# Optimization experiments

Hardware: AMD Instinct MI355X
Metric: run time of the kernel (lower is better)

Reference implementation:

```python
import jax, jax.numpy as jnp
import numpy as np

B, N, F_IN = 2, 2048, 256
HEADS, F_OUT = 8, 32
NEG_SLOPE = 0.01  # torch F.leaky_relu default


def setup_inputs() -> dict:
    key = jax.random.key(0)
    k1, k2, k3, k4 = jax.random.split(key, 4)
    stdv = 1.0 / np.sqrt(F_OUT * HEADS)
    h = jax.random.normal(k1, (B, N, F_IN), dtype=jnp.float32)
    adj = jax.random.uniform(k2, (B, N, N), dtype=jnp.float32)
    W = jax.random.normal(k3, (F_IN, F_OUT * HEADS), dtype=jnp.float32) * stdv
    a = jax.random.normal(k4, (2 * F_OUT, 1), dtype=jnp.float32) * stdv
    return {"h": h, "adj": adj, "W": W, "a": a}


def reference(h, adj, W, a):
    # adj is accepted by the original forward but never used (dense attention).
    b, n, _ = h.shape
    f = a.shape[0] // 2
    heads = W.shape[1] // f
    Wh = (h @ W).reshape(b, n, heads, f)            # [b,n,h,f]
    a1 = a[:f, 0]                                    # attends to source i
    a2 = a[f:, 0]                                    # attends to target j
    e1 = jnp.einsum('bnhf,f->bhn', Wh, a1)           # [b,h,n]
    e2 = jnp.einsum('bnhf,f->bhn', Wh, a2)           # [b,h,n]
    # e[b,h,i,j] = leaky_relu(a1.Wh_i + a2.Wh_j) == a^T [Wh_i || Wh_j]
    e = jax.nn.leaky_relu(e1[:, :, :, None] + e2[:, :, None, :], NEG_SLOPE)
    att = jax.nn.softmax(e, axis=-1)                 # softmax over neighbors j
    h_prime = jnp.einsum('bhij,bjhf->bihf', att, Wh)  # [b,n,h,f]
    return h_prime.reshape(b, n, heads * f)
```

## Files before the change

kernel.cpp:

```cpp
#include <hip/hip_runtime.h>
#include <math.h>

#define BATCH 2
#define NTOK  2048
#define FIN   256
#define HEADS 8
#define FOUT  32
#define BH    (BATCH*HEADS)
#define NCOL  (HEADS*FOUT)
#define ROWS  (BATCH*NTOK)

static const size_t OFF_E1   = 1048576;
static const size_t OFF_E2   = OFF_E1 + 32768;
static const size_t OFF_SKEY = OFF_E2 + 32768;
static const size_t OFF_SIDX = OFF_SKEY + 32768;
static const size_t OFF_W1S  = OFF_SIDX + 32768;
static const size_t OFF_W2S  = OFF_W1S + 32768;
static const size_t OFF_S1   = OFF_W2S + 32768;
static const size_t OFF_P2   = OFF_S1 + 32784;
static const size_t OFF_V1   = OFF_P2 + 32784;
static const size_t OFF_P2V  = OFF_V1 + 16u*2049u*32u;
static const size_t OFF_PART = OFF_V1;

__global__ __launch_bounds__(256) void k_gemm(const float* __restrict__ h,
                                              const float* __restrict__ W,
                                              float* __restrict__ Wh) {
    __shared__ float As[32 * 68];
    __shared__ float Bs[64 * 68];
    const int tid  = threadIdx.x;
    const int row0 = blockIdx.x * 32;
    const int col0 = blockIdx.y * 64;
    const int tc = tid & 15;
    const int tr = tid >> 4;
    const int r0 = tr * 2;

    const float4* h4 = (const float4*)h;
    const float4* W4 = (const float4*)W;

    float4 acc0 = make_float4(0.f,0.f,0.f,0.f);
    float4 acc1 = make_float4(0.f,0.f,0.f,0.f);

    for (int kc = 0; kc < FIN; kc += 64) {
        #pragma unroll
        for (int q = 0; q < 2; ++q) {
            int idx = q * 256 + tid;
            int r  = idx >> 4;
            int kq = idx & 15;
            float4 v = h4[(size_t)(row0 + r) * 64 + (kc >> 2) + kq];
            *(float4*)&As[r * 68 + kq * 4] = v;
        }
        #pragma unroll
        for (int q = 0; q < 4; ++q) {
            int idx = q * 256 + tid;
            int kr = idx >> 4;
            int cf = idx & 15;
            float4 v = W4[(size_t)(kc + kr) * 64 + (col0 >> 2) + cf];
            *(float4*)&Bs[kr * 68 + cf * 4] = v;
        }
        __syncthreads();

        #pragma unroll
        for (int kq = 0; kq < 16; ++kq) {
            float4 af0 = *(const float4*)&As[r0 * 68 + kq * 4];
            float4 af1 = *(const float4*)&As[(r0 + 1) * 68 + kq * 4];
            #pragma unroll
            for (int c = 0; c < 4; ++c) {
                float4 b = *(const float4*)&Bs[(kq * 4 + c) * 68 + tc * 4];
                float a0 = (c == 0) ? af0.x : (c == 1) ? af0.y : (c == 2) ? af0.z : af0.w;
                float a1 = (c == 0) ? af1.x : (c == 1) ? af1.y : (c == 2) ? af1.z : af1.w;
                acc0.x += a0 * b.x; acc0.y += a0 * b.y; acc0.z += a0 * b.z; acc0.w += a0 * b.w;
                acc1.x += a1 * b.x; acc1.y += a1 * b.y; acc1.z += a1 * b.z; acc1.w += a1 * b.w;
            }
        }
        __syncthreads();
    }
    *(float4*)(Wh + (size_t)(row0 + r0)     * NCOL + col0 + tc * 4) = acc0;
    *(float4*)(Wh + (size_t)(row0 + r0 + 1) * NCOL + col0 + tc * 4) = acc1;
}

__global__ __launch_bounds__(256) void k_e12(const float* __restrict__ Wh,
                                             const float* __restrict__ a,
                                             float* __restrict__ e1,
                                             float* __restrict__ e2) {
    __shared__ float av[64];
    const int tid = threadIdx.x;
    if (tid < 64) av[tid] = a[tid];
    __syncthreads();

    const int g     = blockIdx.x * 256 + tid;
    const int n_lin = g >> 3;
    const int hh    = g & 7;
    const float4* p = (const float4*)(Wh + (size_t)n_lin * NCOL + hh * FOUT);
    float s1 = 0.f, s2 = 0.f;
    #pragma unroll
    for (int q = 0; q < 8; ++q) {
        float4 v = p[q];
        s1 += v.x * av[q*4+0] + v.y * av[q*4+1] + v.z * av[q*4+2] + v.w * av[q*4+3];
        s2 += v.x * av[32+q*4+0] + v.y * av[32+q*4+1] + v.z * av[32+q*4+2] + v.w * av[32+q*4+3];
    }
    const int b  = n_lin >> 11;
    const int n  = n_lin & (NTOK - 1);
    const int bh = b * HEADS + hh;
    e1[bh * NTOK + n] = s1;
    e2[bh * NTOK + n] = s2;
}

__global__ __launch_bounds__(256) void k_rank8(const float* __restrict__ e2g,
                                               int* __restrict__ partial) {
    __shared__ float ch[256];
    const int tid = threadIdx.x;
    const int bh  = blockIdx.x;
    const int jt  = blockIdx.y;
    const int kt  = blockIdx.z;
    ch[tid] = e2g[bh * NTOK + kt * 256 + tid];
    __syncthreads();

    const int j    = jt * 256 + tid;
    const float my = e2g[bh * NTOK + j];
    const int base0 = kt * 256;
    int rank = 0;
    const float4* c4 = (const float4*)ch;
    #pragma unroll 8
    for (int q = 0; q < 64; ++q) {
        float4 v = c4[q];
        int bb = base0 + q * 4;
        rank += (v.x > my) || ((v.x == my) && (bb + 0 < j));
        rank += (v.y > my) || ((v.y == my) && (bb + 1 < j));
        rank += (v.z > my) || ((v.z == my) && (bb + 2 < j));
        rank += (v.w > my) || ((v.w == my) && (bb + 3 < j));
    }
    partial[(kt * BH + bh) * NTOK + j] = rank;
}

__global__ __launch_bounds__(256) void k_scatter(const float* __restrict__ e2g,
                                                 const int* __restrict__ partial,
                                                 float* __restrict__ skey,
                                                 int* __restrict__ sidx,
                                                 float* __restrict__ w1s,
                                                 float* __restrict__ w2s) {
    const int tid = threadIdx.x;
    const int bh  = blockIdx.x;
    const int jt  = blockIdx.y;
    const int j   = jt * 256 + tid;
    int rank = 0;
    #pragma unroll
    for (int kt = 0; kt < 8; ++kt)
        rank += partial[(kt * BH + bh) * NTOK + j];
    const float my = e2g[bh * NTOK + j];
    skey[bh * NTOK + rank] = my;
    sidx[bh * NTOK + rank] = j;
    w1s[bh * NTOK + rank]  = expf(my);
    w2s[bh * NTOK + rank]  = expf(0.01f * my);
}

__global__ __launch_bounds__(1024) void k_vscan(const float* __restrict__ Wh,
                                                const int* __restrict__ sidx,
                                                const float* __restrict__ w1s,
                                                const float* __restrict__ w2s,
                                                float* __restrict__ V1,
                                                float* __restrict__ P2V,
                                                float* __restrict__ S1,
                                                float* __restrict__ P2) {
    __shared__ float4 wtot[16];
    __shared__ float4 woff[16];
    const int t    = threadIdx.x;
    const int lane = t & 63;
    const int wv   = t >> 6;
    const int fg   = blockIdx.x;
    const int bh   = blockIdx.y;
    const int z    = blockIdx.z;
    const int b    = bh >> 3;
    const int hh   = bh & 7;
    const float* wsrc = z ? w2s : w1s;

    const int j0 = 2 * t;
    float4 v0, v1;
    if (fg < 8) {
        int sj0 = sidx[bh * NTOK + j0];
        int sj1 = sidx[bh * NTOK + j0 + 1];
        float w0 = wsrc[bh * NTOK + j0];
        float w1 = wsrc[bh * NTOK + j0 + 1];
        float4 g0 = *(const float4*)(Wh + (size_t)(b * NTOK + sj0) * NCOL + hh * FOUT + fg * 4);
        float4 g1 = *(const float4*)(Wh + (size_t)(b * NTOK + sj1) * NCOL + hh * FOUT + fg * 4);
        v0 = make_float4(w0 * g0.x, w0 * g0.y, w0 * g0.z, w0 * g0.w);
        v1 = make_float4(w1 * g1.x, w1 * g1.y, w1 * g1.z, w1 * g1.w);
    } else {
        v0 = make_float4(wsrc[bh * NTOK + j0],     0.f, 0.f, 0.f);
        v1 = make_float4(wsrc[bh * NTOK + j0 + 1], 0.f, 0.f, 0.f);
    }

    float4 s = make_float4(v0.x + v1.x, v0.y + v1.y, v0.z + v1.z, v0.w + v1.w);
    #pragma unroll
    for (int d = 1; d < 64; d <<= 1) {
        float ux = __shfl_up(s.x, (unsigned)d, 64);
        float uy = __shfl_up(s.y, (unsigned)d, 64);
        float uz = __shfl_up(s.z, (unsigned)d, 64);
        float uw = __shfl_up(s.w, (unsigned)d, 64);
        if (lane >= d) { s.x += ux; s.y += uy; s.z += uz; s.w += uw; }
    }
    float4 pair = make_float4(v0.x + v1.x, v0.y + v1.y, v0.z + v1.z, v0.w + v1.w);
    float4 excl = make_float4(s.x - pair.x, s.y - pair.y, s.z - pair.z, s.w - pair.w);
    if (lane == 63) wtot[wv] = s;
    __syncthreads();
    if (t < 16) {
        float4 ws = wtot[t];
        float4 inc = ws;
        #pragma unroll
        for (int d = 1; d < 16; d <<= 1) {
            float ux = __shfl_up(inc.x, (unsigned)d, 16);
            float uy = __shfl_up(inc.y, (unsigned)d, 16);
            float uz = __shfl_up(inc.z, (unsigned)d, 16);
            float uw = __shfl_up(inc.w, (unsigned)d, 16);
            if ((t & 15) >= d) { inc.x += ux; inc.y += uy; inc.z += uz; inc.w += uw; }
        }
        woff[t] = make_float4(inc.x - ws.x, inc.y - ws.y, inc.z - ws.z, inc.w - ws.w);
    }
    __syncthreads();

    float4 base = woff[wv];
    float4 i0 = make_float4(base.x + excl.x + v0.x, base.y + excl.y + v0.y,
                            base.z + excl.z + v0.z, base.w + excl.w + v0.w);
    float4 i1 = make_float4(i0.x + v1.x, i0.y + v1.y, i0.z + v1.z, i0.w + v1.w);

    if (fg < 8) {
        float* dst = z ? P2V : V1;
        *(float4*)(dst + ((size_t)bh * 2049 + (j0 + 1)) * 32 + fg * 4) = i0;
        *(float4*)(dst + ((size_t)bh * 2049 + (j0 + 2)) * 32 + fg * 4) = i1;
        if (t == 0)
            *(float4*)(dst + ((size_t)bh * 2049) * 32 + fg * 4) = make_float4(0.f,0.f,0.f,0.f);
    } else {
        float* dst = z ? P2 : S1;
        dst[bh * 2049 + j0 + 1] = i0.x;
        dst[bh * 2049 + j0 + 2] = i1.x;
        if (t == 0) dst[bh * 2049] = 0.f;
    }
}

__global__ __launch_bounds__(256) void k_out(const float* __restrict__ skey,
                                             const float* __restrict__ e1g,
                                             const float* __restrict__ S1,
                                             const float* __restrict__ P2,
                                             const float* __restrict__ V1,
                                             const float* __restrict__ P2V,
                                             float* __restrict__ out) {
    __shared__ float keys[NTOK];
    const int tid = threadIdx.x;
    const int it  = blockIdx.x;
    const int bh  = blockIdx.y;
    const int b   = bh >> 3;
    const int hh  = bh & 7;
    #pragma unroll
    for (int q = 0; q < 8; ++q)
        keys[q * 256 + tid] = skey[bh * NTOK + q * 256 + tid];
    __syncthreads();

    const int i  = it * 32 + (tid >> 3);
    const int fg = tid & 7;
    const float e1v = e1g[bh * NTOK + i];
    const float th  = -e1v;
    int lo = 0, hi = NTOK;
    while (lo < hi) {
        int mid = (lo + hi) >> 1;
        if (keys[mid] > th) lo = mid + 1; else hi = mid;
    }
    const int k = lo;
    const float A = expf(e1v);
    const float C = expf(0.01f * e1v);
    const float s1  = S1[bh * 2049 + k];
    const float p2k = P2[bh * 2049 + k];
    const float p2t = P2[bh * 2049 + 2048];
    const float l   = A * s1 + C * (p2t - p2k);
    const float inv = 1.0f / l;
    float4 v1   = *(const float4*)(V1  + ((size_t)bh * 2049 + k)    * 32 + fg * 4);
    float4 p2v  = *(const float4*)(P2V + ((size_t)bh * 2049 + k)    * 32 + fg * 4);
    float4 p2vt = *(const float4*)(P2V + ((size_t)bh * 2049 + 2048) * 32 + fg * 4);
    float4 o;
    o.x = (A * v1.x + C * (p2vt.x - p2v.x)) * inv;
    o.y = (A * v1.y + C * (p2vt.y - p2v.y)) * inv;
    o.z = (A * v1.z + C * (p2vt.z - p2v.z)) * inv;
    o.w = (A * v1.w + C * (p2vt.w - p2v.w)) * inv;
    *(float4*)(out + (size_t)(b * NTOK + i) * NCOL + hh * FOUT + fg * 4) = o;
}

extern "C" void kernel_launch(void* const* d_in, const int* in_sizes, int n_in,
                              void* d_out, int out_size, void* d_ws, size_t ws_size,
                              hipStream_t stream) {
    const float* h = (const float*)d_in[0];
    const float* W = (const float*)d_in[2];
    const float* a = (const float*)d_in[3];
    float* out = (float*)d_out;
    float* ws  = (float*)d_ws;

    float* Wh   = ws;
    float* e1   = ws + OFF_E1;
    float* e2   = ws + OFF_E2;
    float* skey = ws + OFF_SKEY;
    int*   sidx = (int*)(ws + OFF_SIDX);
    float* w1s  = ws + OFF_W1S;
    float* w2s  = ws + OFF_W2S;
    float* S1   = ws + OFF_S1;
    float* P2   = ws + OFF_P2;
    float* V1   = ws + OFF_V1;
    float* P2V  = ws + OFF_P2V;
    int*   part = (int*)(ws + OFF_PART);

    k_gemm   <<<dim3(ROWS / 32, NCOL / 64), 256, 0, stream>>>(h, W, Wh);
    k_e12    <<<dim3(ROWS * HEADS / 256),   256, 0, stream>>>(Wh, a, e1, e2);
    k_rank8  <<<dim3(BH, 8, 8),             256, 0, stream>>>(e2, part);
    k_scatter<<<dim3(BH, 8),                256, 0, stream>>>(e2, part, skey, sidx, w1s, w2s);
    k_vscan  <<<dim3(9, BH, 2),            1024, 0, stream>>>(Wh, sidx, w1s, w2s, V1, P2V, S1, P2);
    k_out    <<<dim3(NTOK / 32, BH),        256, 0, stream>>>(skey, e1, S1, P2, V1, P2V, out);
}
```

Baseline: 126.9 us.

## Double-buffer 64x64 GEMM tiles, use packed 64-bit sort keys, split prefix planes

The projection GEMM now uses 64x64 output tiles with a 4x4 register micro-tile per thread, a transposed A tile in shared memory and double-buffered register prefetch. This raises arithmetic reuse and halves the number of barriers per k-step. The rank kernel packs each float key and its index into one order-preserving 64-bit integer, so every comparison is a single compare instead of a compare plus tie-break. The V1/P2V prefix arrays are stored as per-feature-group planes, which changes the gather pattern in the output kernel. The risks are more register pressure and 64-bit compare cost in the rank loop.

New measurement: 122.1 us. -3.8%, faster.

```diff
diff --git a/kernel.cpp b/kernel.cpp
--- a/kernel.cpp
+++ b/kernel.cpp
@@ -25,57 +25,67 @@
 __global__ __launch_bounds__(256) void k_gemm(const float* __restrict__ h,
                                               const float* __restrict__ W,
                                               float* __restrict__ Wh) {
-    __shared__ float As[32 * 68];
-    __shared__ float Bs[64 * 68];
+    __shared__ alignas(16) float As[2][32][68];
+    __shared__ alignas(16) float Bs[2][32][72];
     const int tid  = threadIdx.x;
-    const int row0 = blockIdx.x * 32;
+    const int row0 = blockIdx.x * 64;
     const int col0 = blockIdx.y * 64;
-    const int tc = tid & 15;
-    const int tr = tid >> 4;
-    const int r0 = tr * 2;
-
-    const float4* h4 = (const float4*)h;
-    const float4* W4 = (const float4*)W;
+    const int tx   = tid & 15;
+    const int ty   = tid >> 4;
+    const int ar   = tid >> 3;
+    const int akq  = tid & 7;
+    const int bkr  = tid >> 4;
+    const int bcf  = tid & 15;
+    const int colf = col0 >> 2;
+
+    const float4* __restrict__ h4 = (const float4*)h;
+    const float4* __restrict__ W4 = (const float4*)W;
+
+    float4 a0 = h4[(size_t)(row0 + ar)      * 64 + akq];
+    float4 a1 = h4[(size_t)(row0 + 32 + ar) * 64 + akq];
+    float4 b0 = W4[(size_t)(bkr)      * 64 + colf + bcf];
+    float4 b1 = W4[(size_t)(16 + bkr) * 64 + colf + bcf];
 
     float4 acc0 = make_float4(0.f,0.f,0.f,0.f);
     float4 acc1 = make_float4(0.f,0.f,0.f,0.f);
-
-    for (int kc = 0; kc < FIN; kc += 64) {
-        #pragma unroll
-        for (int q = 0; q < 2; ++q) {
-            int idx = q * 256 + tid;
-            int r  = idx >> 4;
-            int kq = idx & 15;
-            float4 v = h4[(size_t)(row0 + r) * 64 + (kc >> 2) + kq];
-            *(float4*)&As[r * 68 + kq * 4] = v;
+    float4 acc2 = make_float4(0.f,0.f,0.f,0.f);
+    float4 acc3 = make_float4(0.f,0.f,0.f,0.f);
+
+    for (int t = 0; t < FIN / 32; ++t) {
+        const int cur = t & 1;
+        As[cur][akq*4+0][ar]      = a0.x;
+        As[cur][akq*4+1][ar]      = a0.y;
+        As[cur][akq*4+2][ar]      = a0.z;
+        As[cur][akq*4+3][ar]      = a0.w;
+        As[cur][akq*4+0][32 + ar] = a1.x;
+        As[cur][akq*4+1][32 + ar] = a1.y;
+        As[cur][akq*4+2][32 + ar] = a1.z;
+        As[cur][akq*4+3][32 + ar] = a1.w;
+        *(float4*)&Bs[cur][bkr][bcf*4]      = b0;
+        *(float4*)&Bs[cur][16 + bkr][bcf*4] = b1;
+        __syncthreads();
+        if (t + 1 < FIN / 32) {
+            const int kc = (t + 1) * 32;
+            a0 = h4[(size_t)(row0 + ar)      * 64 + (kc >> 2) + akq];
+            a1 = h4[(size_t)(row0 + 32 + ar) * 64 + (kc >> 2) + akq];
+            b0 = W4[(size_t)(kc + bkr)      * 64 + colf + bcf];
+            b1 = W4[(size_t)(kc + 16 + bkr) * 64 + colf + bcf];
         }
         #pragma unroll
-        for (int q = 0; q < 4; ++q) {
-            int idx = q * 256 + tid;
-            int kr = idx >> 4;
-            int cf = idx & 15;
-            float4 v = W4[(size_t)(kc + kr) * 64 + (col0 >> 2) + cf];
-            *(float4*)&Bs[kr * 68 + cf * 4] = v;
+        for (int k = 0; k < 32; ++k) {
+            float4 a4 = *(const float4*)&As[cur][k][ty*4];
+            float4 b4 = *(const float4*)&Bs[cur][k][tx*4];
+            acc0.x += a4.x*b4.x; acc0.y += a4.x*b4.y; acc0.z += a4.x*b4.z; acc0.w += a4.x*b4.w;
+            acc1.x += a4.y*b4.x; acc1.y += a4.y*b4.y; acc1.z += a4.y*b4.z; acc1.w += a4.y*b4.w;
+            acc2.x += a4.z*b4.x; acc2.y += a4.z*b4.y; acc2.z += a4.z*b4.z; acc2.w += a4.z*b4.w;
+            acc3.x += a4.w*b4.x; acc3.y += a4.w*b4.y; acc3.z += a4.w*b4.z; acc3.w += a4.w*b4.w;
         }
-        __syncthreads();
-
-        #pragma unroll
-        for (int kq = 0; kq < 16; ++kq) {
-            float4 af0 = *(const float4*)&As[r0 * 68 + kq * 4];
-            float4 af1 = *(const float4*)&As[(r0 + 1) * 68 + kq * 4];
-            #pragma unroll
-            for (int c = 0; c < 4; ++c) {
-                float4 b = *(const float4*)&Bs[(kq * 4 + c) * 68 + tc * 4];
-                float a0 = (c == 0) ? af0.x : (c == 1) ? af0.y : (c == 2) ? af0.z : af0.w;
-                float a1 = (c == 0) ? af1.x : (c == 1) ? af1.y : (c == 2) ? af1.z : af1.w;
-                acc0.x += a0 * b.x; acc0.y += a0 * b.y; acc0.z += a0 * b.z; acc0.w += a0 * b.w;
-                acc1.x += a1 * b.x; acc1.y += a1 * b.y; acc1.z += a1 * b.z; acc1.w += a1 * b.w;
-            }
-        }
-        __syncthreads();
-    }
-    *(float4*)(Wh + (size_t)(row0 + r0)     * NCOL + col0 + tc * 4) = acc0;
-    *(float4*)(Wh + (size_t)(row0 + r0 + 1) * NCOL + col0 + tc * 4) = acc1;
+    }
+    const int orow = row0 + ty*4;
+    *(float4*)(Wh + (size_t)(orow + 0) * NCOL + col0 + tx*4) = acc0;
+    *(float4*)(Wh + (size_t)(orow + 1) * NCOL + col0 + tx*4) = acc1;
+    *(float4*)(Wh + (size_t)(orow + 2) * NCOL + col0 + tx*4) = acc2;
+    *(float4*)(Wh + (size_t)(orow + 3) * NCOL + col0 + tx*4) = acc3;
 }
 
 __global__ __launch_bounds__(256) void k_e12(const float* __restrict__ Wh,
@@ -105,29 +115,32 @@
     e2[bh * NTOK + n] = s2;
 }
 
+__device__ __forceinline__ unsigned long long sortkey(float f, int j) {
+    unsigned int b = __float_as_uint(f);
+    unsigned int u = (b & 0x80000000u) ? ~b : (b | 0x80000000u);
+    return ((unsigned long long)u << 32) | (unsigned int)(NTOK - 1 - j);
+}
+
 __global__ __launch_bounds__(256) void k_rank8(const float* __restrict__ e2g,
                                                int* __restrict__ partial) {
-    __shared__ float ch[256];
+    __shared__ alignas(16) unsigned long long ch[256];
     const int tid = threadIdx.x;
     const int bh  = blockIdx.x;
     const int jt  = blockIdx.y;
     const int kt  = blockIdx.z;
-    ch[tid] = e2g[bh * NTOK + kt * 256 + tid];
-    __syncthreads();
-
-    const int j    = jt * 256 + tid;
-    const float my = e2g[bh * NTOK + j];
-    const int base0 = kt * 256;
+    const int kbase = kt * 256;
+    ch[tid] = sortkey(e2g[bh * NTOK + kbase + tid], kbase + tid);
+    __syncthreads();
+
+    const int j = jt * 256 + tid;
+    const unsigned long long my = sortkey(e2g[bh * NTOK + j], j);
     int rank = 0;
-    const float4* c4 = (const float4*)ch;
+    const ulonglong2* c2 = (const ulonglong2*)ch;
     #pragma unroll 8
-    for (int q = 0; q < 64; ++q) {
-        float4 v = c4[q];
-        int bb = base0 + q * 4;
-        rank += (v.x > my) || ((v.x == my) && (bb + 0 < j));
-        rank += (v.y > my) || ((v.y == my) && (bb + 1 < j));
-        rank += (v.z > my) || ((v.z == my) && (bb + 2 < j));
-        rank += (v.w > my) || ((v.w == my) && (bb + 3 < j));
+    for (int q = 0; q < 128; ++q) {
+        ulonglong2 v = c2[q];
+        rank += (v.x > my);
+        rank += (v.y > my);
     }
     partial[(kt * BH + bh) * NTOK + j] = rank;
 }
@@ -224,10 +237,11 @@
 
     if (fg < 8) {
         float* dst = z ? P2V : V1;
-        *(float4*)(dst + ((size_t)bh * 2049 + (j0 + 1)) * 32 + fg * 4) = i0;
-        *(float4*)(dst + ((size_t)bh * 2049 + (j0 + 2)) * 32 + fg * 4) = i1;
+        float* plane = dst + ((size_t)bh * 8 + fg) * (2049u * 4u);
+        *(float4*)(plane + (size_t)(j0 + 1) * 4) = i0;
+        *(float4*)(plane + (size_t)(j0 + 2) * 4) = i1;
         if (t == 0)
-            *(float4*)(dst + ((size_t)bh * 2049) * 32 + fg * 4) = make_float4(0.f,0.f,0.f,0.f);
+            *(float4*)plane = make_float4(0.f,0.f,0.f,0.f);
     } else {
         float* dst = z ? P2 : S1;
         dst[bh * 2049 + j0 + 1] = i0.x;
@@ -271,9 +285,11 @@
     const float p2t = P2[bh * 2049 + 2048];
     const float l   = A * s1 + C * (p2t - p2k);
     const float inv = 1.0f / l;
-    float4 v1   = *(const float4*)(V1  + ((size_t)bh * 2049 + k)    * 32 + fg * 4);
-    float4 p2v  = *(const float4*)(P2V + ((size_t)bh * 2049 + k)    * 32 + fg * 4);
-    float4 p2vt = *(const float4*)(P2V + ((size_t)bh * 2049 + 2048) * 32 + fg * 4);
+    const float* v1p  = V1  + ((size_t)bh * 8 + fg) * (2049u * 4u);
+    const float* p2vp = P2V + ((size_t)bh * 8 + fg) * (2049u * 4u);
+    float4 v1   = *(const float4*)(v1p  + (size_t)k * 4);
+    float4 p2v  = *(const float4*)(p2vp + (size_t)k * 4);
+    float4 p2vt = *(const float4*)(p2vp + (size_t)2048 * 4);
     float4 o;
     o.x = (A * v1.x + C * (p2vt.x - p2v.x)) * inv;
     o.y = (A * v1.y + C * (p2vt.y - p2v.y)) * inv;
@@ -304,7 +320,7 @@
     float* P2V  = ws + OFF_P2V;
     int*   part = (int*)(ws + OFF_PART);
 
-    k_gemm   <<<dim3(ROWS / 32, NCOL / 64), 256, 0, stream>>>(h, W, Wh);
+    k_gemm   <<<dim3(ROWS / 64, NCOL / 64), 256, 0, stream>>>(h, W, Wh);
     k_e12    <<<dim3(ROWS * HEADS / 256),   256, 0, stream>>>(Wh, a, e1, e2);
     k_rank8  <<<dim3(BH, 8, 8),             256, 0, stream>>>(e2, part);
     k_scatter<<<dim3(BH, 8),                256, 0, stream>>>(e2, part, skey, sidx, w1s, w2s);
```
